# Performance work log

Hardware: AMD Instinct MI355X
Metric: run time of the kernel (lower is better)

Reference implementation:

```python
import jax, jax.numpy as jnp
import numpy as np

N, E = 20000, 640000
LATENT, HID, OUT, HEADS = 512, 256, 128, 2
NEG_SLOPE = 0.2


def setup_inputs() -> dict:
    key = jax.random.key(0)
    ks = jax.random.split(key, 12)
    s = 0.02
    return {
        "z": jax.random.normal(ks[0], (N, LATENT), dtype=jnp.float32),
        "edge_index": jax.random.randint(ks[1], (2, E), 0, N, dtype=jnp.int64),
        "W1": jax.random.normal(ks[2], (LATENT, HID), dtype=jnp.float32) * s,
        "b1": jnp.zeros((HID,), dtype=jnp.float32),
        "W2": jax.random.normal(ks[3], (HID, HID * HEADS), dtype=jnp.float32) * s,
        "b2": jnp.zeros((HID * HEADS,), dtype=jnp.float32),
        "Wg": jax.random.normal(ks[4], (HID * HEADS, HEADS * OUT), dtype=jnp.float32) * s,
        "att_src": jax.random.normal(ks[5], (HEADS, OUT), dtype=jnp.float32) * s,
        "att_dst": jax.random.normal(ks[6], (HEADS, OUT), dtype=jnp.float32) * s,
        "bias_g": jnp.zeros((HEADS * OUT,), dtype=jnp.float32),
        "W3": jax.random.normal(ks[7], (OUT * HEADS, 512), dtype=jnp.float32) * s,
        "b3": jnp.zeros((512,), dtype=jnp.float32),
    }


def _gat_conv(x, edge_index, Wg, att_src, att_dst, bias_g):
    n = x.shape[0]
    # add self loops (PyG GATConv default add_self_loops=True)
    loops = jnp.tile(jnp.arange(n, dtype=edge_index.dtype)[None, :], (2, 1))
    ei = jnp.concatenate([edge_index, loops], axis=1)
    src, dst = ei[0], ei[1]
    xp = (x @ Wg).reshape(n, HEADS, OUT)          # [N,H,C]
    a_src = jnp.einsum('nhc,hc->nh', xp, att_src)  # [N,H]
    a_dst = jnp.einsum('nhc,hc->nh', xp, att_dst)
    alpha = jax.nn.leaky_relu(a_src[src] + a_dst[dst], NEG_SLOPE)  # [E+N,H]
    amax = jax.ops.segment_max(alpha, dst, num_segments=n)
    alpha = jnp.exp(alpha - amax[dst])
    denom = jax.ops.segment_sum(alpha, dst, num_segments=n)
    alpha = alpha / jnp.maximum(denom[dst], 1e-16)
    msg = xp[src] * alpha[:, :, None]              # [E+N,H,C]
    out = jax.ops.segment_sum(msg, dst, num_segments=n)  # [N,H,C]
    return out.reshape(n, HEADS * OUT) + bias_g


def reference(z, edge_index, W1, b1, W2, b2, Wg, att_src, att_dst, bias_g, W3, b3):
    x = jax.nn.relu(z @ W1 + b1)
    x = jax.nn.relu(x @ W2 + b2)
    x = _gat_conv(x, edge_index, Wg, att_src, att_dst, bias_g)
    return x @ W3 + b3
```

## Files before the change

kernel.cpp:

```cpp
#include <hip/hip_runtime.h>
#include <hip/hip_bf16.h>
#include <float.h>

#define N_NODES 20000
#define LATENT  512
#define HID     256
#define OUT_C   128
#define HEADS   2
#define HC      256
#define NEG_SLOPE 0.2f

typedef _Float16 half8 __attribute__((ext_vector_type(8)));
typedef __attribute__((ext_vector_type(4))) float f32x4;

__device__ __forceinline__ ushort f2h(float v) {
    _Float16 h = (_Float16)v;
    return *(ushort*)&h;
}
__device__ __forceinline__ float h2f(ushort u) {
    _Float16 h = *(_Float16*)&u;
    return (float)h;
}

__device__ __forceinline__ void gl_lds16(const ushort* g, ushort* l) {
    __builtin_amdgcn_global_load_lds(
        (const __attribute__((address_space(1))) unsigned int*)g,
        (__attribute__((address_space(3))) unsigned int*)l, 16, 0, 0);
}

template<int BN>
__global__ __launch_bounds__(256) void gemm_f16(
    const ushort* __restrict__ A, const ushort* __restrict__ BT,
    const float* __restrict__ bias,
    float* __restrict__ Cf, ushort* __restrict__ Ch,
    int M, int N, int K, int relu)
{
    constexpr int NI  = BN / 32;
    constexpr int BUF = 4096 + BN * 32;
    __shared__ ushort lds[2 * BUF];
    ushort* buf0 = lds;
    ushort* buf1 = lds + BUF;

    const int t = threadIdx.x;
    const int l = t & 63;
    const int w = t >> 6;
    const int wm = (w >> 1) * 64;
    const int wn = (w & 1) * (BN / 2);
    const int lm = l & 15;
    const int q  = l >> 4;
    const int q4 = q * 4;

    const int row0 = blockIdx.x * 128;
    const int col0 = blockIdx.y * BN;

    const int jr0 = w * 16 + (l >> 2);
    const int gsh = (((l & 3) ^ ((l >> 4) & 3)) << 3);
    const ushort* gA0 = A + (size_t)(row0 + jr0) * K + gsh;
    const ushort* gA1 = gA0 + (size_t)64 * K;
    const ushort* gB0 = BT + (size_t)(col0 + jr0) * K + gsh;
    const ushort* gB1 = gB0 + (size_t)64 * K;
    const int dA0 = w * 512, dA1 = (4 + w) * 512;
    const int dB0 = 4096 + w * 512, dB1 = 4096 + (4 + w) * 512;

    const int csw = ((q ^ ((lm >> 2) & 3)) << 3);

    const f32x4 zf = {0.f, 0.f, 0.f, 0.f};
    f32x4 acc[4][NI];
    #pragma unroll
    for (int i = 0; i < 4; ++i)
        #pragma unroll
        for (int j = 0; j < NI; ++j) acc[i][j] = zf;

    auto issue = [&](int kk, ushort* B) {
        gl_lds16(gA0 + kk, B + dA0);
        gl_lds16(gA1 + kk, B + dA1);
        gl_lds16(gB0 + kk, B + dB0);
        if (BN == 128) gl_lds16(gB1 + kk, B + dB1);
    };

    auto compute = [&](const ushort* B) {
        half8 bf[NI];
        #pragma unroll
        for (int ni = 0; ni < NI; ++ni) {
            const int boff = (wn + ni * 16 + lm) * 32 + csw;
            bf[ni] = *(const half8*)&B[4096 + boff];
        }
        #pragma unroll
        for (int mi = 0; mi < 4; ++mi) {
            const int aoff = (wm + mi * 16 + lm) * 32 + csw;
            half8 af = *(const half8*)&B[aoff];
            #pragma unroll
            for (int ni = 0; ni < NI; ++ni)
                acc[mi][ni] = __builtin_amdgcn_mfma_f32_16x16x32_f16(
                    af, bf[ni], acc[mi][ni], 0, 0, 0);
        }
    };

    issue(0, buf0);
    __syncthreads();
    for (int k0 = 0; k0 < K; k0 += 64) {
        issue(k0 + 32, buf1);
        compute(buf0);
        __syncthreads();
        if (k0 + 64 < K) issue(k0 + 64, buf0);
        compute(buf1);
        __syncthreads();
    }

    #pragma unroll
    for (int mi = 0; mi < 4; ++mi) {
        #pragma unroll
        for (int ni = 0; ni < NI; ++ni) {
            const int col = col0 + wn + ni * 16 + lm;
            const float bv = bias ? bias[col] : 0.f;
            #pragma unroll
            for (int r = 0; r < 4; ++r) {
                const int row = row0 + wm + mi * 16 + q4 + r;
                if (row >= M) continue;
                float v = acc[mi][ni][r] + bv;
                if (relu) v = fmaxf(v, 0.f);
                const size_t idx = (size_t)row * N + col;
                if (Cf) Cf[idx] = v;
                if (Ch) Ch[idx] = f2h(v);
            }
        }
    }
}

__global__ __launch_bounds__(256) void cvt_zero_kernel(
    const float* __restrict__ x, ushort* __restrict__ o, int n4,
    int* deg, int* cursor, int n)
{
    int i = blockIdx.x * 256 + threadIdx.x;
    if (i < n) { deg[i] = 0; cursor[i] = 0; }
    if (i >= n4) return;
    float4 v = ((const float4*)x)[i];
    ((ushort4*)o)[i] = make_ushort4(f2h(v.x), f2h(v.y), f2h(v.z), f2h(v.w));
}

__global__ __launch_bounds__(256) void transpose_cvt4_kernel(
    const float* __restrict__ W1, const float* __restrict__ W2,
    const float* __restrict__ Wg, const float* __restrict__ W3,
    ushort* __restrict__ T1, ushort* __restrict__ T2,
    ushort* __restrict__ Tg, ushort* __restrict__ T3)
{
    int idx = blockIdx.x * 256 + threadIdx.x;
    int which = idx >> 17, i = idx & 131071;
    const float* W; ushort* T; int K, N;
    if (which == 0)      { W = W1; T = T1; K = 512; N = 256; }
    else if (which == 1) { W = W2; T = T2; K = 256; N = 512; }
    else if (which == 2) { W = Wg; T = Tg; K = 512; N = 256; }
    else                 { W = W3; T = T3; K = 256; N = 512; }
    int k = i / N, n = i - k * N;
    T[(size_t)n * K + k] = f2h(W[i]);
}

__global__ __launch_bounds__(256) void att_kernel(
    const ushort* __restrict__ xp, const float* __restrict__ att_src,
    const float* __restrict__ att_dst,
    float* __restrict__ a_src, float* __restrict__ a_dst, int n)
{
    int node = (blockIdx.x * 256 + threadIdx.x) >> 6;
    int lane = threadIdx.x & 63;
    if (node >= n) return;
    int h = lane >> 5, lh = lane & 31;
    int c = h * OUT_C + lh * 4;
    const ushort4 v = *(const ushort4*)(xp + (size_t)node * HC + c);
    const float4 as = *(const float4*)(att_src + c);
    const float4 ad = *(const float4*)(att_dst + c);
    float x0 = h2f(v.x), x1 = h2f(v.y), x2 = h2f(v.z), x3 = h2f(v.w);
    float s1 = x0 * as.x + x1 * as.y + x2 * as.z + x3 * as.w;
    float s2 = x0 * ad.x + x1 * ad.y + x2 * ad.z + x3 * ad.w;
    #pragma unroll
    for (int off = 16; off > 0; off >>= 1) {
        s1 += __shfl_xor(s1, off);
        s2 += __shfl_xor(s2, off);
    }
    if (lh == 0) { a_src[2 * node + h] = s1; a_dst[2 * node + h] = s2; }
}

__global__ __launch_bounds__(256) void hist_kernel(
    const int* __restrict__ dst, int* deg, int E_real, int ET)
{
    int e = blockIdx.x * blockDim.x + threadIdx.x;
    if (e >= ET) return;
    int d = (e < E_real) ? dst[e] : (e - E_real);
    atomicAdd(&deg[d], 1);
}

__global__ __launch_bounds__(1024) void scan_kernel(
    const int* __restrict__ deg, int* __restrict__ rowptr, int n)
{
    __shared__ int part[1024];
    const int t = threadIdx.x;
    const int chunk = (n + 1023) / 1024;
    const int lo = t * chunk;
    const int hi = min(lo + chunk, n);
    int s = 0;
    for (int i = lo; i < hi; ++i) s += deg[i];
    part[t] = s;
    __syncthreads();
    #pragma unroll
    for (int off = 1; off < 1024; off <<= 1) {
        int add = (t >= off) ? part[t - off] : 0;
        __syncthreads();
        part[t] += add;
        __syncthreads();
    }
    int run = part[t] - s;
    for (int i = lo; i < hi; ++i) { rowptr[i] = run; run += deg[i]; }
    if (t == 1023) rowptr[n] = part[1023];
}

__global__ __launch_bounds__(256) void scatter_kernel(
    const int* __restrict__ src, const int* __restrict__ dst,
    const int* __restrict__ rowptr, int* cursor,
    int* __restrict__ sorted_src, int E_real, int ET)
{
    int e = blockIdx.x * blockDim.x + threadIdx.x;
    if (e >= ET) return;
    int s, d;
    if (e < E_real) { s = src[e]; d = dst[e]; }
    else            { s = e - E_real; d = s; }
    int pos = rowptr[d] + atomicAdd(&cursor[d], 1);
    sorted_src[pos] = s;
}

__global__ __launch_bounds__(256) void gat_aggregate(
    const int* __restrict__ rowptr, const int* __restrict__ sorted_src,
    const float* __restrict__ a_src, const float* __restrict__ a_dst,
    const ushort* __restrict__ xp, const float* __restrict__ bias_g,
    ushort* __restrict__ xg, int n)
{
    const int d = blockIdx.x * 4 + (threadIdx.x >> 6);
    if (d >= n) return;
    const int lane = threadIdx.x & 63;
    const int h = lane >> 5;
    const int start = rowptr[d], end = rowptr[d + 1];

    const float ad0 = a_dst[2 * d + 0];
    const float ad1 = a_dst[2 * d + 1];

    float4 acc = make_float4(0.f, 0.f, 0.f, 0.f);
    float denom = 0.f;

    for (int e0 = start; e0 < end; e0 += 64) {
        const int cnt = min(64, end - e0);
        float w0 = 0.f, w1 = 0.f;
        int off = 0;
        if (lane < cnt) {
            int s = sorted_src[e0 + lane];
            float v0 = a_src[2 * s + 0] + ad0;
            float v1 = a_src[2 * s + 1] + ad1;
            v0 = (v0 > 0.f) ? v0 : NEG_SLOPE * v0;
            v1 = (v1 > 0.f) ? v1 : NEG_SLOPE * v1;
            w0 = __expf(v0);
            w1 = __expf(v1);
            off = s * HC;
        }
        for (int j = 0; j < cnt; ++j) {
            const float wa = __shfl(w0, j);
            const float wb = __shfl(w1, j);
            const float w  = h ? wb : wa;
            const int   o  = __shfl(off, j);
            const ushort4 v = *(const ushort4*)(xp + o + 4 * lane);
            denom += w;
            acc.x += w * h2f(v.x); acc.y += w * h2f(v.y);
            acc.z += w * h2f(v.z); acc.w += w * h2f(v.w);
        }
    }

    const float inv = 1.f / fmaxf(denom, 1e-16f);
    const int c = 4 * lane;
    const float4 bg = *(const float4*)(bias_g + c);
    const size_t base = ((size_t)d * HC + c) >> 2;
    ((ushort4*)xg)[base] = make_ushort4(
        f2h(acc.x * inv + bg.x), f2h(acc.y * inv + bg.y),
        f2h(acc.z * inv + bg.z), f2h(acc.w * inv + bg.w));
}

extern "C" void kernel_launch(void* const* d_in, const int* in_sizes, int n_in,
                              void* d_out, int out_size, void* d_ws, size_t ws_size,
                              hipStream_t stream)
{
    const float* z       = (const float*)d_in[0];
    const int*   ei      = (const int*)d_in[1];
    const float* W1      = (const float*)d_in[2];
    const float* b1      = (const float*)d_in[3];
    const float* W2      = (const float*)d_in[4];
    const float* b2      = (const float*)d_in[5];
    const float* Wg      = (const float*)d_in[6];
    const float* att_src = (const float*)d_in[7];
    const float* att_dst = (const float*)d_in[8];
    const float* bias_g  = (const float*)d_in[9];
    const float* W3      = (const float*)d_in[10];
    const float* b3      = (const float*)d_in[11];
    float* out = (float*)d_out;

    const int n = N_NODES;
    const int E_real = in_sizes[1] / 2;
    const int ET = E_real + n;
    const int* src = ei;
    const int* dst = ei + E_real;

    char* p = (char*)d_ws;
    auto alloc = [&](size_t bytes) {
        char* r = p;
        p += (bytes + 63) & ~(size_t)63;
        return r;
    };
    const int np = n + 128;
    ushort* z_f16  = (ushort*)alloc((size_t)np * LATENT * 2);
    ushort* x1_f16 = (ushort*)alloc((size_t)np * HID * 2);
    ushort* xp_f16 = (ushort*)alloc((size_t)n * HC * 2);
    ushort* W1T = (ushort*)alloc((size_t)LATENT * HID * 2);
    ushort* W2T = (ushort*)alloc((size_t)HID * 512 * 2);
    ushort* WgT = (ushort*)alloc((size_t)512 * HC * 2);
    ushort* W3T = (ushort*)alloc((size_t)HC * 512 * 2);
    float* a_src = (float*)alloc((size_t)2 * n * 4);
    float* a_dst = (float*)alloc((size_t)2 * n * 4);
    int* deg        = (int*)alloc((size_t)n * 4);
    int* rowptr     = (int*)alloc(((size_t)n + 1) * 4);
    int* cursor     = (int*)alloc((size_t)n * 4);
    int* sorted_src = (int*)alloc((size_t)ET * 4);
    ushort* x2_f16 = z_f16;
    ushort* xg_f16 = x1_f16;

    const int gm128 = (n + 127) / 128;

    cvt_zero_kernel<<<(n * LATENT / 4 + 255) / 256, 256, 0, stream>>>(
        z, z_f16, n * LATENT / 4, deg, cursor, n);
    transpose_cvt4_kernel<<<(4 * 131072) / 256, 256, 0, stream>>>(
        W1, W2, Wg, W3, W1T, W2T, WgT, W3T);

    gemm_f16<64><<<dim3(gm128, HID / 64), 256, 0, stream>>>(
        z_f16, W1T, b1, nullptr, x1_f16, n, HID, LATENT, 1);
    gemm_f16<64><<<dim3(gm128, 512 / 64), 256, 0, stream>>>(
        x1_f16, W2T, b2, nullptr, x2_f16, n, 512, HID, 1);
    gemm_f16<64><<<dim3(gm128, HC / 64), 256, 0, stream>>>(
        x2_f16, WgT, nullptr, nullptr, xp_f16, n, HC, 512, 0);

    att_kernel<<<(n * 64 + 255) / 256, 256, 0, stream>>>(
        xp_f16, att_src, att_dst, a_src, a_dst, n);
    hist_kernel<<<(ET + 255) / 256, 256, 0, stream>>>(dst, deg, E_real, ET);
    scan_kernel<<<1, 1024, 0, stream>>>(deg, rowptr, n);
    scatter_kernel<<<(ET + 255) / 256, 256, 0, stream>>>(
        src, dst, rowptr, cursor, sorted_src, E_real, ET);
    gat_aggregate<<<(n + 3) / 4, 256, 0, stream>>>(
        rowptr, sorted_src, a_src, a_dst, xp_f16, bias_g, xg_f16, n);

    gemm_f16<64><<<dim3(gm128, 512 / 64), 256, 0, stream>>>(
        xg_f16, W3T, b3, out, nullptr, n, 512, HC, 0);
}
```

Baseline: 345.4 us.

## Deepen GEMM LDS pipeline to four buffers and unroll GAT gather loop

The GEMM moves from a double-buffered loop with two block barriers per 64-K step to a four-slot ring that keeps three chunks in flight. Explicit vmcnt waits and a single barrier per chunk replace the old syncs, and the BN=128 path is removed by a static_assert. The GAT aggregation kernel now processes edges in groups of 32. Lanes in each half compute only their own head's weight, and the inner loop is unrolled by four so that four row gathers are issued before they are accumulated. This trades more LDS use and hardcoded wait counts for better latency hiding in both kernels.

```diff
diff --git a/kernel.cpp b/kernel.cpp
--- a/kernel.cpp
+++ b/kernel.cpp
@@ -35,11 +35,10 @@
     float* __restrict__ Cf, ushort* __restrict__ Ch,
     int M, int N, int K, int relu)
 {
+    static_assert(BN == 64, "vmcnt immediates assume 3 DMAs/chunk");
     constexpr int NI  = BN / 32;
     constexpr int BUF = 4096 + BN * 32;
-    __shared__ ushort lds[2 * BUF];
-    ushort* buf0 = lds;
-    ushort* buf1 = lds + BUF;
+    __shared__ ushort lds[4 * BUF];
 
     const int t = threadIdx.x;
     const int l = t & 63;
@@ -58,9 +57,8 @@
     const ushort* gA0 = A + (size_t)(row0 + jr0) * K + gsh;
     const ushort* gA1 = gA0 + (size_t)64 * K;
     const ushort* gB0 = BT + (size_t)(col0 + jr0) * K + gsh;
-    const ushort* gB1 = gB0 + (size_t)64 * K;
     const int dA0 = w * 512, dA1 = (4 + w) * 512;
-    const int dB0 = 4096 + w * 512, dB1 = 4096 + (4 + w) * 512;
+    const int dB0 = 4096 + w * 512;
 
     const int csw = ((q ^ ((lm >> 2) & 3)) << 3);
 
@@ -71,14 +69,18 @@
         #pragma unroll
         for (int j = 0; j < NI; ++j) acc[i][j] = zf;
 
-    auto issue = [&](int kk, ushort* B) {
+    const int NC = K >> 5;
+
+    auto issue = [&](int c) {
+        ushort* B = lds + (size_t)(c & 3) * BUF;
+        const int kk = c * 32;
         gl_lds16(gA0 + kk, B + dA0);
         gl_lds16(gA1 + kk, B + dA1);
         gl_lds16(gB0 + kk, B + dB0);
-        if (BN == 128) gl_lds16(gB1 + kk, B + dB1);
     };
 
-    auto compute = [&](const ushort* B) {
+    auto compute = [&](int c) {
+        const ushort* B = lds + (size_t)(c & 3) * BUF;
         half8 bf[NI];
         #pragma unroll
         for (int ni = 0; ni < NI; ++ni) {
@@ -96,15 +98,16 @@
         }
     };
 
-    issue(0, buf0);
-    __syncthreads();
-    for (int k0 = 0; k0 < K; k0 += 64) {
-        issue(k0 + 32, buf1);
-        compute(buf0);
-        __syncthreads();
-        if (k0 + 64 < K) issue(k0 + 64, buf0);
-        compute(buf1);
-        __syncthreads();
+    issue(0); issue(1); issue(2);
+    for (int c = 0; c < NC; ++c) {
+        const int ahead = min(NC - 1 - c, 2);
+        if (ahead == 2)      asm volatile("s_waitcnt vmcnt(6)" ::: "memory");
+        else if (ahead == 1) asm volatile("s_waitcnt vmcnt(3)" ::: "memory");
+        else                 asm volatile("s_waitcnt vmcnt(0)" ::: "memory");
+        __builtin_amdgcn_s_barrier();
+        __builtin_amdgcn_sched_barrier(0);
+        if (c + 3 < NC) issue(c + 3);
+        compute(c);
     }
 
     #pragma unroll
@@ -235,7 +238,7 @@
     const int d = blockIdx.x * 4 + (threadIdx.x >> 6);
     if (d >= n) return;
     const int lane = threadIdx.x & 63;
-    const int h = lane >> 5;
+    const int hsel = lane & 32;
     const int start = rowptr[d], end = rowptr[d + 1];
 
     const float ad0 = a_dst[2 * d + 0];
@@ -244,25 +247,43 @@
     float4 acc = make_float4(0.f, 0.f, 0.f, 0.f);
     float denom = 0.f;
 
-    for (int e0 = start; e0 < end; e0 += 64) {
-        const int cnt = min(64, end - e0);
-        float w0 = 0.f, w1 = 0.f;
-        int off = 0;
-        if (lane < cnt) {
-            int s = sorted_src[e0 + lane];
+    for (int e0 = start; e0 < end; e0 += 32) {
+        const int cnt = min(32, end - e0);
+        const int idx = lane & 31;
+        float wsel = 0.f; int off = 0;
+        if (idx < cnt) {
+            int s = sorted_src[e0 + idx];
             float v0 = a_src[2 * s + 0] + ad0;
             float v1 = a_src[2 * s + 1] + ad1;
             v0 = (v0 > 0.f) ? v0 : NEG_SLOPE * v0;
             v1 = (v1 > 0.f) ? v1 : NEG_SLOPE * v1;
-            w0 = __expf(v0);
-            w1 = __expf(v1);
+            wsel = (lane < 32) ? __expf(v0) : __expf(v1);
             off = s * HC;
         }
-        for (int j = 0; j < cnt; ++j) {
-            const float wa = __shfl(w0, j);
-            const float wb = __shfl(w1, j);
-            const float w  = h ? wb : wa;
-            const int   o  = __shfl(off, j);
+        int j = 0;
+        for (; j + 4 <= cnt; j += 4) {
+            float w_[4]; int o_[4];
+            #pragma unroll
+            for (int u = 0; u < 4; ++u) {
+                w_[u] = __shfl(wsel, (j + u) + hsel);
+                o_[u] = __shfl(off, j + u);
+            }
+            ushort4 v_[4];
+            #pragma unroll
+            for (int u = 0; u < 4; ++u)
+                v_[u] = *(const ushort4*)(xp + o_[u] + 4 * lane);
+            #pragma unroll
+            for (int u = 0; u < 4; ++u) {
+                denom += w_[u];
+                acc.x += w_[u] * h2f(v_[u].x);
+                acc.y += w_[u] * h2f(v_[u].y);
+                acc.z += w_[u] * h2f(v_[u].z);
+                acc.w += w_[u] * h2f(v_[u].w);
+            }
+        }
+        for (; j < cnt; ++j) {
+            const float w = __shfl(wsel, j + hsel);
+            const int   o = __shfl(off, j);
             const ushort4 v = *(const ushort4*)(xp + o + 4 * lane);
             denom += w;
             acc.x += w * h2f(v.x); acc.y += w * h2f(v.y);
```

Measured after the change: 342.2 us. No clear change (-0.9%).
